# Optimization experiments

Hardware: AMD Instinct MI355X
Metric: run time of the kernel (lower is better)

The kernel has to match this reference:

```python
import jax, jax.numpy as jnp
import numpy as np

N_HEAD = 16
LORA_DIM = 16
LORA_ALPHA = 32


def setup_inputs() -> dict:
    key = jax.random.key(0)
    ks = jax.random.split(key, 8)
    B, S, D = 2, 2048, 1024
    std = 0.02
    return {
        "x": jax.random.normal(ks[0], (B, S, D), jnp.float32),
        "c_attn_w": jax.random.normal(ks[1], (D, 3 * D), jnp.float32) * std,
        "c_attn_b": jnp.zeros((3 * D,), jnp.float32),
        "c_proj_w": jax.random.normal(ks[2], (D, D), jnp.float32) * std,
        "c_proj_b": jnp.zeros((D,), jnp.float32),
        "q_a1": jax.random.normal(ks[3], (D, LORA_DIM), jnp.float32) * std,
        "q_a2": jax.random.normal(ks[4], (LORA_DIM, D), jnp.float32) * std,
        "v_a1": jax.random.normal(ks[5], (D, LORA_DIM), jnp.float32) * std,
        "v_a2": jax.random.normal(ks[6], (LORA_DIM, D), jnp.float32) * std,
    }


def reference(x, c_attn_w, c_attn_b, c_proj_w, c_proj_b, q_a1, q_a2, v_a1, v_a2):
    B, S, D = x.shape
    H = N_HEAD
    hd = D // H
    # NOTE: original code uses adapter_dim / adapter_alpha as the scale
    lora_scale = jnp.float32(LORA_DIM / LORA_ALPHA)

    qkv = x @ c_attn_w + c_attn_b                      # [B,S,3D]
    q, k, v = jnp.split(qkv, 3, axis=-1)
    q = q + ((x @ q_a1) @ q_a2) * lora_scale
    v = v + ((x @ v_a1) @ v_a2) * lora_scale

    def heads(t):
        return t.reshape(B, S, H, hd).transpose(0, 2, 1, 3)  # [B,H,S,hd]

    qh, kh, vh = heads(q), heads(k), heads(v)

    w = jnp.einsum('bhqd,bhkd->bhqk', qh, kh) / jnp.sqrt(jnp.float32(hd))
    bias = jnp.tril(jnp.ones((S, S), dtype=w.dtype))   # causal mask
    w = w * bias - jnp.float32(1e10) * (1 - bias)
    w = jax.nn.softmax(w, axis=-1)
    a = jnp.einsum('bhqk,bhkd->bhqd', w, vh)
    a = a.transpose(0, 2, 1, 3).reshape(B, S, D)       # merge heads
    a = a @ c_proj_w + c_proj_b

    present = jnp.stack((kh, vh))                      # [2,B,H,S,hd]
    return a, present
```

## Files before the change

### kernel.cpp

```cpp
#include <hip/hip_runtime.h>

#define T_TOK 4096
#define D_DIM 1024
#define N3    3072
#define S_LEN 2048
#define NH    16
#define HD    64
#define KAUG  1056

#define OUT_A_ELEMS   4194304
#define OUT_KV_ELEMS  4194304

typedef __attribute__((ext_vector_type(8))) short bf16x8;
typedef __attribute__((ext_vector_type(4))) float f32x4;
typedef __attribute__((ext_vector_type(16))) float f32x16;
typedef _Float16 f16x8 __attribute__((ext_vector_type(8)));
typedef _Float16 f16x4 __attribute__((ext_vector_type(4)));

union U4 { unsigned u[4]; bf16x8 v; };

#define GHASH(r) ((((r) >> 1) ^ ((r) >> 3)) & 3)

__device__ __forceinline__ unsigned short f2bf(float f) {
    unsigned u = __float_as_uint(f);
    u += 0x7FFFu + ((u >> 16) & 1u);
    return (unsigned short)(u >> 16);
}
__device__ __forceinline__ float bf2f(unsigned short h) {
    return __uint_as_float(((unsigned)h) << 16);
}
__device__ __forceinline__ unsigned cvtpk(float a, float b) {
    unsigned r;
    asm("v_cvt_pk_bf16_f32 %0, %1, %2" : "=v"(r) : "v"(a), "v"(b));
    return r;
}

#define GLL16(gp, lp) __builtin_amdgcn_global_load_lds( \
    (const __attribute__((address_space(1))) unsigned int*)(gp), \
    (__attribute__((address_space(3))) unsigned int*)(lp), 16, 0, 0)

#define MFMA32(A, B, C) __builtin_amdgcn_mfma_f32_32x32x16_bf16(A, B, C, 0, 0, 0)
#define MFMA16F(A, B, C) __builtin_amdgcn_mfma_f32_16x16x32_f16(A, B, C, 0, 0, 0)

__global__ __launch_bounds__(256) void lora1_v2(const float* __restrict__ x,
    const float* __restrict__ qa1, const float* __restrict__ va1,
    float* __restrict__ tq, float* __restrict__ tv) {
    int tid = threadIdx.x;
    int w = tid >> 6;
    int lane = tid & 63;
    int t = blockIdx.x * 4 + w;
    int cg = lane & 7;
    int ks = lane >> 3;
    const float* a1 = (cg < 4) ? qa1 : va1;
    int c4 = (cg & 3) * 4;
    const float* xr = x + (size_t)t * D_DIM + ks * 128;
    const float* ar = a1 + (size_t)(ks * 128) * 16 + c4;
    float4 acc = make_float4(0.f, 0.f, 0.f, 0.f);
#pragma unroll 8
    for (int j = 0; j < 128; ++j) {
        float xv = xr[j];
        float4 av = *(const float4*)&ar[j * 16];
        acc.x = fmaf(xv, av.x, acc.x);
        acc.y = fmaf(xv, av.y, acc.y);
        acc.z = fmaf(xv, av.z, acc.z);
        acc.w = fmaf(xv, av.w, acc.w);
    }
#pragma unroll
    for (int m = 8; m < 64; m <<= 1) {
        acc.x += __shfl_xor(acc.x, m);
        acc.y += __shfl_xor(acc.y, m);
        acc.z += __shfl_xor(acc.z, m);
        acc.w += __shfl_xor(acc.w, m);
    }
    if (lane < 8) {
        float* dst = (cg < 4) ? &tq[t * 16 + c4] : &tv[t * 16 + (cg - 4) * 4];
        *(float4*)dst = acc;
    }
}

__global__ __launch_bounds__(256) void splitA_f16(const float* __restrict__ x,
    const float* __restrict__ tq, const float* __restrict__ tv,
    _Float16* __restrict__ af) {
    int idx = blockIdx.x * 256 + threadIdx.x;
    const int total = T_TOK * (KAUG / 4);
    if (idx >= total) return;
    int t = idx / (KAUG / 4);
    int c4 = (idx - t * (KAUG / 4)) * 4;
    float4 v;
    if (c4 < D_DIM)           v = *(const float4*)&x[(size_t)t * D_DIM + c4];
    else if (c4 < D_DIM + 16) v = *(const float4*)&tq[t * 16 + (c4 - D_DIM)];
    else                      v = *(const float4*)&tv[t * 16 + (c4 - D_DIM - 16)];
    f16x4 h;
    h[0] = (_Float16)v.x; h[1] = (_Float16)v.y;
    h[2] = (_Float16)v.z; h[3] = (_Float16)v.w;
    *(f16x4*)&af[(size_t)t * KAUG + c4] = h;
}

__global__ __launch_bounds__(256) void splitW_f16(const float* __restrict__ w,
    const float* __restrict__ qa2, const float* __restrict__ va2,
    _Float16* __restrict__ bf) {
    __shared__ float T[32][65];
    int bn = blockIdx.x;
    int bk = blockIdx.y;
    int tid = threadIdx.x;
#pragma unroll
    for (int u = 0; u < 2; ++u) {
        int id = tid + 256 * u;
        int kr = id >> 4;
        int n4 = (id & 15) * 4;
        int k = bk * 32 + kr;
        int n = bn * 64 + n4;
        float4 v = make_float4(0.f, 0.f, 0.f, 0.f);
        if (k < D_DIM) {
            v = *(const float4*)&w[(size_t)k * N3 + n];
        } else if (k < D_DIM + 16) {
            if (n < D_DIM) {
                float4 q4 = *(const float4*)&qa2[(k - D_DIM) * D_DIM + n];
                v = make_float4(q4.x * 0.5f, q4.y * 0.5f, q4.z * 0.5f, q4.w * 0.5f);
            }
        } else {
            if (n >= 2 * D_DIM) {
                float4 q4 = *(const float4*)&va2[(k - D_DIM - 16) * D_DIM + (n - 2 * D_DIM)];
                v = make_float4(q4.x * 0.5f, q4.y * 0.5f, q4.z * 0.5f, q4.w * 0.5f);
            }
        }
        T[kr][n4 + 0] = v.x; T[kr][n4 + 1] = v.y;
        T[kr][n4 + 2] = v.z; T[kr][n4 + 3] = v.w;
    }
    __syncthreads();
    int n = tid >> 2;
    int k8 = (tid & 3) * 8;
    f16x8 hv;
#pragma unroll
    for (int j = 0; j < 8; ++j) hv[j] = (_Float16)T[k8 + j][n];
    int nr = bn * 64 + n;
    int gsw = (tid & 3) ^ GHASH(nr);
    size_t ro = (size_t)nr * KAUG + bk * 32 + gsw * 8;
    *(f16x8*)&bf[ro] = hv;
}

__global__ __launch_bounds__(256) void wprep_f16(const float* __restrict__ w,
    _Float16* __restrict__ bf) {
    __shared__ float T[32][65];
    int bn = blockIdx.x;
    int bk = blockIdx.y;
    int tid = threadIdx.x;
#pragma unroll
    for (int u = 0; u < 2; ++u) {
        int id = tid + 256 * u;
        int kr = id >> 4;
        int n4 = (id & 15) * 4;
        float4 v = *(const float4*)&w[(size_t)(bk * 32 + kr) * D_DIM + bn * 64 + n4];
        T[kr][n4 + 0] = v.x; T[kr][n4 + 1] = v.y;
        T[kr][n4 + 2] = v.z; T[kr][n4 + 3] = v.w;
    }
    __syncthreads();
    int n = tid >> 2;
    int k8 = (tid & 3) * 8;
    f16x8 hv;
#pragma unroll
    for (int j = 0; j < 8; ++j) hv[j] = (_Float16)T[k8 + j][n];
    int nr = bn * 64 + n;
    int gsw = (tid & 3) ^ GHASH(nr);
    size_t ro = (size_t)nr * D_DIM + bk * 32 + gsw * 8;
    *(f16x8*)&bf[ro] = hv;
}

__global__ __launch_bounds__(256, 3) void qkv_mfma(
    const _Float16* __restrict__ a_g, const _Float16* __restrict__ b_g,
    const float* __restrict__ bias,
    float* __restrict__ qstage, float* __restrict__ pres) {
    __shared__ _Float16 Bf[2][128 * 32];
    int id = blockIdx.y * 24 + blockIdx.x;
    int nid = (id & 7) * 96 + (id >> 3);
    int bn = nid % 24;
    int bm = nid / 24;
    int tid = threadIdx.x;
    int w = tid >> 6, l = tid & 63;
    int wr = w >> 1, wc = w & 1;

    f32x4 acc[4][4];
#pragma unroll
    for (int i = 0; i < 4; ++i)
#pragma unroll
        for (int j = 0; j < 4; ++j)
            acc[i][j] = (f32x4){0.f, 0.f, 0.f, 0.f};

    int srow = l >> 2;
    int sk = (l & 3) * 8;
    const size_t b_base0 = (size_t)(bn * 128 + w * 32 + srow) * KAUG + sk;
    const size_t b_base1 = b_base0 + (size_t)16 * KAUG;
    const int ldso0 = (w * 32) * 32;
    const int ldso1 = (w * 32 + 16) * 32;

    int lrow = l & 15;
    int lg = l >> 4;

    const _Float16* aF[4];
#pragma unroll
    for (int i = 0; i < 4; ++i) {
        int row = bm * 128 + wr * 64 + i * 16 + lrow;
        aF[i] = a_g + (size_t)row * KAUG + lg * 8;
    }
    int roB[4];
#pragma unroll
    for (int j = 0; j < 4; ++j) {
        int Rb = wc * 64 + j * 16 + lrow;
        roB[j] = Rb * 32 + ((lg ^ GHASH(Rb)) * 8);
    }

    f16x8 cA[4], nA[4];

    GLL16(b_g + b_base0, &Bf[0][ldso0]);
    GLL16(b_g + b_base1, &Bf[0][ldso1]);
#pragma unroll
    for (int i = 0; i < 4; ++i) cA[i] = *(const f16x8*)(aF[i]);
    asm volatile("s_waitcnt vmcnt(0)" ::: "memory");
    __builtin_amdgcn_s_barrier();

    const int NT = KAUG / 32;
    for (int t = 0; t < NT; ++t) {
        int cur = t & 1;
        if (t + 1 < NT) {
            int kn = (t + 1) * 32;
            GLL16(b_g + b_base0 + kn, &Bf[cur ^ 1][ldso0]);
            GLL16(b_g + b_base1 + kn, &Bf[cur ^ 1][ldso1]);
            __builtin_amdgcn_sched_barrier(0);
#pragma unroll
            for (int i = 0; i < 4; ++i) nA[i] = *(const f16x8*)(aF[i] + kn);
        }
        f16x8 fb[4];
#pragma unroll
        for (int j = 0; j < 4; ++j) fb[j] = *(const f16x8*)&Bf[cur][roB[j]];
#pragma unroll
        for (int i = 0; i < 4; ++i)
#pragma unroll
            for (int j = 0; j < 4; ++j)
                acc[i][j] = MFMA16F(cA[i], fb[j], acc[i][j]);
        if (t + 1 < NT) {
            asm volatile("s_waitcnt vmcnt(4)" ::: "memory");
            __builtin_amdgcn_s_barrier();
#pragma unroll
            for (int i = 0; i < 4; ++i) cA[i] = nA[i];
        }
    }

    int seg = bn >> 3;
#pragma unroll
    for (int j = 0; j < 4; ++j) {
        int n = bn * 128 + wc * 64 + j * 16 + lrow;
        float bz = bias[n];
        int h = (n >> 6) & 15;
        int d = n & 63;
#pragma unroll
        for (int i = 0; i < 4; ++i) {
            int tbase = bm * 128 + wr * 64 + i * 16 + (l >> 4) * 4;
#pragma unroll
            for (int r = 0; r < 4; ++r) {
                int t = tbase + r;
                float v = acc[i][j][r] + bz;
                int bb = t >> 11, s = t & 2047;
                size_t idx = (((size_t)(bb * NH + h) * S_LEN + s) * HD) + d;
                if (seg == 0)      qstage[idx] = v * 0.125f;
                else if (seg == 1) pres[idx] = v;
                else               pres[OUT_KV_ELEMS + idx] = v;
            }
        }
    }
}

__global__ __launch_bounds__(256, 3) void proj_mfma(
    const _Float16* __restrict__ a_g, const _Float16* __restrict__ b_g,
    const float* __restrict__ bias, float* __restrict__ outp) {
    __shared__ _Float16 Bf[2][128 * 32];
    int id = blockIdx.y * 8 + blockIdx.x;
    int nid = (id & 7) * 32 + (id >> 3);
    int bn = nid % 8;
    int bm = nid / 8;
    int tid = threadIdx.x;
    int w = tid >> 6, l = tid & 63;
    int wr = w >> 1, wc = w & 1;

    f32x4 acc[4][4];
#pragma unroll
    for (int i = 0; i < 4; ++i)
#pragma unroll
        for (int j = 0; j < 4; ++j)
            acc[i][j] = (f32x4){0.f, 0.f, 0.f, 0.f};

    int srow = l >> 2;
    int sk = (l & 3) * 8;
    const size_t b_base0 = (size_t)(bn * 128 + w * 32 + srow) * D_DIM + sk;
    const size_t b_base1 = b_base0 + (size_t)16 * D_DIM;
    const int ldso0 = (w * 32) * 32;
    const int ldso1 = (w * 32 + 16) * 32;

    int lrow = l & 15;
    int lg = l >> 4;

    const _Float16* aF[4];
#pragma unroll
    for (int i = 0; i < 4; ++i) {
        int row = bm * 128 + wr * 64 + i * 16 + lrow;
        aF[i] = a_g + (size_t)row * D_DIM + lg * 8;
    }
    int roB[4];
#pragma unroll
    for (int j = 0; j < 4; ++j) {
        int Rb = wc * 64 + j * 16 + lrow;
        roB[j] = Rb * 32 + ((lg ^ GHASH(Rb)) * 8);
    }

    f16x8 cA[4], nA[4];

    GLL16(b_g + b_base0, &Bf[0][ldso0]);
    GLL16(b_g + b_base1, &Bf[0][ldso1]);
#pragma unroll
    for (int i = 0; i < 4; ++i) cA[i] = *(const f16x8*)(aF[i]);
    asm volatile("s_waitcnt vmcnt(0)" ::: "memory");
    __builtin_amdgcn_s_barrier();

    const int NT = D_DIM / 32;
    for (int t = 0; t < NT; ++t) {
        int cur = t & 1;
        if (t + 1 < NT) {
            int kn = (t + 1) * 32;
            GLL16(b_g + b_base0 + kn, &Bf[cur ^ 1][ldso0]);
            GLL16(b_g + b_base1 + kn, &Bf[cur ^ 1][ldso1]);
            __builtin_amdgcn_sched_barrier(0);
#pragma unroll
            for (int i = 0; i < 4; ++i) nA[i] = *(const f16x8*)(aF[i] + kn);
        }
        f16x8 fb[4];
#pragma unroll
        for (int j = 0; j < 4; ++j) fb[j] = *(const f16x8*)&Bf[cur][roB[j]];
#pragma unroll
        for (int i = 0; i < 4; ++i)
#pragma unroll
            for (int j = 0; j < 4; ++j)
                acc[i][j] = MFMA16F(cA[i], fb[j], acc[i][j]);
        if (t + 1 < NT) {
            asm volatile("s_waitcnt vmcnt(4)" ::: "memory");
            __builtin_amdgcn_s_barrier();
#pragma unroll
            for (int i = 0; i < 4; ++i) cA[i] = nA[i];
        }
    }

#pragma unroll
    for (int j = 0; j < 4; ++j) {
        int n = bn * 128 + wc * 64 + j * 16 + lrow;
        float bz = bias[n];
#pragma unroll
        for (int i = 0; i < 4; ++i) {
            int tbase = bm * 128 + wr * 64 + i * 16 + (l >> 4) * 4;
#pragma unroll
            for (int r = 0; r < 4; ++r)
                outp[(size_t)(tbase + r) * D_DIM + n] = acc[i][j][r] + bz;
        }
    }
}

__global__ __launch_bounds__(256) void kprep_kernel(const float* __restrict__ kin,
    unsigned short* __restrict__ khp, unsigned short* __restrict__ klp) {
    int id = blockIdx.x * 256 + threadIdx.x;
    int rowi = id >> 3;
    int gsrc = id & 7;
    const float* src = kin + (size_t)rowi * 64 + gsrc * 8;
    float4 v0 = *(const float4*)src;
    float4 v1 = *(const float4*)(src + 4);
    int key = rowi & 2047;
    int gp = gsrc ^ (key & 7);
    size_t dst = (size_t)rowi * 64 + gp * 8;
    float vv[8] = {v0.x, v0.y, v0.z, v0.w, v1.x, v1.y, v1.z, v1.w};
    bf16x8 h, lo;
#pragma unroll
    for (int j = 0; j < 8; ++j) {
        unsigned short hh = f2bf(vv[j]);
        h[j] = (short)hh;
        lo[j] = (short)f2bf(vv[j] - bf2f(hh));
    }
    *(bf16x8*)&khp[dst] = h;
    *(bf16x8*)&klp[dst] = lo;
}

__global__ __launch_bounds__(256) void vtprep_kernel(const float* __restrict__ vin,
    unsigned short* __restrict__ vth, unsigned short* __restrict__ vtl) {
    __shared__ __align__(16) unsigned short Th[64][72];
    __shared__ __align__(16) unsigned short Tl[64][72];
    int bh = blockIdx.x;
    int kv0 = blockIdx.y * 64;
    int tid = threadIdx.x;
#pragma unroll
    for (int p = 0; p < 4; ++p) {
        int key = (tid >> 4) + 16 * p;
        int d0 = (tid & 15) * 4;
        float4 v = *(const float4*)&vin[((size_t)bh * 2048 + kv0 + key) * 64 + d0];
        float vv[4] = {v.x, v.y, v.z, v.w};
#pragma unroll
        for (int j = 0; j < 4; ++j) {
            unsigned short hh = f2bf(vv[j]);
            Th[d0 + j][key] = hh;
            Tl[d0 + j][key] = f2bf(vv[j] - bf2f(hh));
        }
    }
    __syncthreads();
    int d = tid >> 2;
#pragma unroll
    for (int q = 0; q < 2; ++q) {
        int gg = (tid & 3) + 4 * q;
        int gs = gg ^ (d & 7);
        bf16x8 hv = *(const bf16x8*)&Th[d][gs * 8];
        bf16x8 lv = *(const bf16x8*)&Tl[d][gs * 8];
        size_t dst = ((size_t)bh * 64 + d) * 2048 + kv0 + gg * 8;
        *(bf16x8*)&vth[dst] = hv;
        *(bf16x8*)&vtl[dst] = lv;
    }
}

__device__ __forceinline__ void stage_tile(
    const unsigned short* __restrict__ kh, const unsigned short* __restrict__ kl,
    const unsigned short* __restrict__ vh, const unsigned short* __restrict__ vl,
    unsigned short (*ldsb)[4096], int w, int l, int bh, int kv0) {
    if (w < 2) {
        const unsigned short* gp = (w == 0 ? kh : kl)
            + ((size_t)bh * 2048 + kv0 + (l >> 3)) * 64 + (l & 7) * 8;
        unsigned short* lp = ldsb[w];
#pragma unroll
        for (int i = 0; i < 8; ++i)
            GLL16(gp + i * 512, lp + i * 512);
    } else {
        const unsigned short* gp = (w == 2 ? vh : vl)
            + ((size_t)bh * 64 + (l >> 3)) * 2048 + kv0 + (l & 7) * 8;
        unsigned short* lp = ldsb[w];
#pragma unroll
        for (int i = 0; i < 8; ++i)
            GLL16(gp + (size_t)i * 16384, lp + i * 512);
    }
}

#define QROW(r) ((((r) & 3) + 8 * ((r) >> 2)) + 4 * g)

__global__ __launch_bounds__(256, 2) void attn_mfma(
    const float* __restrict__ q_s,
    const unsigned short* __restrict__ kh, const unsigned short* __restrict__ kl,
    const unsigned short* __restrict__ vh, const unsigned short* __restrict__ vl,
    _Float16* __restrict__ aout) {
    __shared__ __align__(16) unsigned short lds[2][4][4096];
    int bh = blockIdx.x;
    int qi = (int)gridDim.y - 1 - blockIdx.y;
    int tid = threadIdx.x;
    int w = tid >> 6, l = tid & 63;
    int qloc = l & 31, g = l >> 5;
    int q0 = qi * 128;
    int qg = q0 + w * 32 + qloc;

    bf16x8 qf[4];
    {
        const float* qrow = q_s + ((size_t)bh * S_LEN + qg) * HD;
#pragma unroll
        for (int t = 0; t < 4; ++t) {
            float4 u0 = *(const float4*)&qrow[t * 16 + g * 8];
            float4 u1 = *(const float4*)&qrow[t * 16 + g * 8 + 4];
            float vv[8] = {u0.x, u0.y, u0.z, u0.w, u1.x, u1.y, u1.z, u1.w};
            bf16x8 r;
#pragma unroll
            for (int j = 0; j < 8; ++j) r[j] = (short)f2bf(vv[j]);
            qf[t] = r;
        }
    }

    f32x16 o0, o1;
#pragma unroll
    for (int r = 0; r < 16; ++r) { o0[r] = 0.f; o1[r] = 0.f; }
    float m_run = -1e30f, l_run = 0.f;

    int nt = 2 * qi + 2;
    int qwmax = q0 + w * 32 + 31;

    stage_tile(kh, kl, vh, vl, lds[0], w, l, bh, 0);
    __syncthreads();

    for (int t = 0; t < nt; ++t) {
        int kv0 = t * 64;
        int bi = t & 1;
        if (t + 1 < nt)
            stage_tile(kh, kl, vh, vl, lds[bi ^ 1], w, l, bh, (t + 1) * 64);

        if (kv0 <= qwmax) {
            const unsigned short* Khp = lds[bi][0];
            const unsigned short* Klp = lds[bi][1];
            const unsigned short* Vhp = lds[bi][2];
            const unsigned short* Vlp = lds[bi][3];

            f32x16 s0, s1;
#pragma unroll
            for (int r = 0; r < 16; ++r) { s0[r] = 0.f; s1[r] = 0.f; }

            __builtin_amdgcn_s_setprio(1);
#pragma unroll
            for (int tt = 0; tt < 4; ++tt) {
                int gr = ((2 * tt + g) ^ (qloc & 7)) * 8;
                bf16x8 a0h = *(const bf16x8*)&Khp[qloc * 64 + gr];
                bf16x8 a1h = *(const bf16x8*)&Khp[(32 + qloc) * 64 + gr];
                bf16x8 a0l = *(const bf16x8*)&Klp[qloc * 64 + gr];
                bf16x8 a1l = *(const bf16x8*)&Klp[(32 + qloc) * 64 + gr];
                s0 = MFMA32(a0h, qf[tt], s0);
                s0 = MFMA32(a0l, qf[tt], s0);
                s1 = MFMA32(a1h, qf[tt], s1);
                s1 = MFMA32(a1l, qf[tt], s1);
            }
            __builtin_amdgcn_s_setprio(0);

            if (kv0 + 63 > q0 + w * 32) {
#pragma unroll
                for (int r = 0; r < 16; ++r) {
                    int kk = kv0 + QROW(r);
                    if (kk > qg)      s0[r] = -1e30f;
                    if (kk + 32 > qg) s1[r] = -1e30f;
                }
            }

            float mx = s0[0];
#pragma unroll
            for (int r = 1; r < 16; ++r) mx = fmaxf(mx, s0[r]);
#pragma unroll
            for (int r = 0; r < 16; ++r) mx = fmaxf(mx, s1[r]);
            mx = fmaxf(mx, __shfl_xor(mx, 32));
            float mnew = fmaxf(m_run, mx);
            float al = __expf(m_run - mnew);
            m_run = mnew;
            float rs = 0.f;
#pragma unroll
            for (int r = 0; r < 16; ++r) { s0[r] = __expf(s0[r] - mnew); rs += s0[r]; }
#pragma unroll
            for (int r = 0; r < 16; ++r) { s1[r] = __expf(s1[r] - mnew); rs += s1[r]; }
            rs += __shfl_xor(rs, 32);
            l_run = l_run * al + rs;
#pragma unroll
            for (int r = 0; r < 16; ++r) {
                float ar = __shfl(al, QROW(r));
                o0[r] *= ar; o1[r] *= ar;
            }

            __builtin_amdgcn_s_setprio(1);
#pragma unroll
            for (int ks = 0; ks < 4; ++ks) {
                const int b = (ks & 1) * 8;
                unsigned w0, w1, w2, w3;
                if (ks < 2) {
                    w0 = cvtpk(s0[b + 0], s0[b + 1]);
                    w1 = cvtpk(s0[b + 2], s0[b + 3]);
                    w2 = cvtpk(s0[b + 4], s0[b + 5]);
                    w3 = cvtpk(s0[b + 6], s0[b + 7]);
                } else {
                    w0 = cvtpk(s1[b + 0], s1[b + 1]);
                    w1 = cvtpk(s1[b + 2], s1[b + 3]);
                    w2 = cvtpk(s1[b + 4], s1[b + 5]);
                    w3 = cvtpk(s1[b + 6], s1[b + 7]);
                }
                asm("v_permlane32_swap_b32 %0, %1" : "+v"(w0), "+v"(w2));
                asm("v_permlane32_swap_b32 %0, %1" : "+v"(w1), "+v"(w3));
                U4 u; u.u[0] = w0; u.u[1] = w1; u.u[2] = w2; u.u[3] = w3;
                bf16x8 pa = u.v;
                int gr = ((2 * ks + g) ^ (qloc & 7)) * 8;
                bf16x8 v0h = *(const bf16x8*)&Vhp[qloc * 64 + gr];
                bf16x8 v1h = *(const bf16x8*)&Vhp[(32 + qloc) * 64 + gr];
                bf16x8 v0l = *(const bf16x8*)&Vlp[qloc * 64 + gr];
                bf16x8 v1l = *(const bf16x8*)&Vlp[(32 + qloc) * 64 + gr];
                o0 = MFMA32(pa, v0h, o0);
                o0 = MFMA32(pa, v0l, o0);
                o1 = MFMA32(pa, v1h, o1);
                o1 = MFMA32(pa, v1l, o1);
            }
            __builtin_amdgcn_s_setprio(0);
        }
        __syncthreads();
    }

    int bb = bh >> 4, h = bh & 15;
#pragma unroll
    for (int r = 0; r < 16; ++r) {
        float li = __shfl(l_run, QROW(r));
        float inv = 1.f / li;
        int qq = q0 + w * 32 + QROW(r);
        size_t base = ((size_t)(bb * S_LEN + qq)) * D_DIM + h * HD + qloc;
        aout[base]      = (_Float16)(o0[r] * inv);
        aout[base + 32] = (_Float16)(o1[r] * inv);
    }
}

#define LSTR 68
__global__ __launch_bounds__(256) void attn_kernel(const float* __restrict__ q_s,
    const float* __restrict__ k_s, const float* __restrict__ v_s,
    float* __restrict__ a_s) {
    __shared__ float Qt[64][LSTR];
    __shared__ float KP[64][LSTR];
    __shared__ float Vs[64][LSTR];
    int bh = blockIdx.x;
    int qi = 31 - blockIdx.y;
    int tid = threadIdx.x;
    int tx = tid & 15, ty = tid >> 4;

#pragma unroll
    for (int qq = 0; qq < 4; ++qq) {
        int q  = qq * 16 + (tid >> 4);
        int d4 = (tid & 15) * 4;
        float4 v = *(const float4*)&q_s[((size_t)bh * S_LEN + qi * 64 + q) * HD + d4];
        Qt[d4 + 0][q] = v.x; Qt[d4 + 1][q] = v.y;
        Qt[d4 + 2][q] = v.z; Qt[d4 + 3][q] = v.w;
    }

    float o[4][4];
#pragma unroll
    for (int r = 0; r < 4; ++r)
#pragma unroll
        for (int c = 0; c < 4; ++c) o[r][c] = 0.f;
    float mrow[4] = {-1e30f, -1e30f, -1e30f, -1e30f};
    float lrow[4] = {0.f, 0.f, 0.f, 0.f};

    for (int kt = 0; kt <= qi; ++kt) {
        __syncthreads();
#pragma unroll
        for (int kk2 = 0; kk2 < 4; ++kk2) {
            int k  = kk2 * 16 + (tid >> 4);
            int d4 = (tid & 15) * 4;
            size_t rowoff = ((size_t)bh * S_LEN + kt * 64 + k) * HD + d4;
            float4 kv4 = *(const float4*)&k_s[rowoff];
            KP[d4 + 0][k] = kv4.x; KP[d4 + 1][k] = kv4.y;
            KP[d4 + 2][k] = kv4.z; KP[d4 + 3][k] = kv4.w;
            float4 vv4 = *(const float4*)&v_s[rowoff];
            *(float4*)&Vs[k][d4] = vv4;
        }
        __syncthreads();

        float s[4][4];
#pragma unroll
        for (int r = 0; r < 4; ++r)
#pragma unroll
            for (int c = 0; c < 4; ++c) s[r][c] = 0.f;
#pragma unroll 8
        for (int d = 0; d < 64; ++d) {
            float4 qv = *(const float4*)&Qt[d][ty * 4];
            float4 kv = *(const float4*)&KP[d][tx * 4];
            float qa[4] = {qv.x, qv.y, qv.z, qv.w};
            float ka[4] = {kv.x, kv.y, kv.z, kv.w};
#pragma unroll
            for (int r = 0; r < 4; ++r)
#pragma unroll
                for (int c = 0; c < 4; ++c)
                    s[r][c] = fmaf(qa[r], ka[c], s[r][c]);
        }
        if (kt == qi) {
#pragma unroll
            for (int r = 0; r < 4; ++r)
#pragma unroll
                for (int c = 0; c < 4; ++c)
                    if (tx * 4 + c > ty * 4 + r) s[r][c] = -1e30f;
        }
        __syncthreads();

        float p[4][4];
#pragma unroll
        for (int r = 0; r < 4; ++r) {
            float mx = fmaxf(fmaxf(s[r][0], s[r][1]), fmaxf(s[r][2], s[r][3]));
            mx = fmaxf(mx, __shfl_xor(mx, 1));
            mx = fmaxf(mx, __shfl_xor(mx, 2));
            mx = fmaxf(mx, __shfl_xor(mx, 4));
            mx = fmaxf(mx, __shfl_xor(mx, 8));
            float mn = fmaxf(mrow[r], mx);
            float alpha = __expf(mrow[r] - mn);
            mrow[r] = mn;
            float rsum = 0.f;
#pragma unroll
            for (int c = 0; c < 4; ++c) {
                p[r][c] = __expf(s[r][c] - mn);
                rsum += p[r][c];
            }
            rsum += __shfl_xor(rsum, 1);
            rsum += __shfl_xor(rsum, 2);
            rsum += __shfl_xor(rsum, 4);
            rsum += __shfl_xor(rsum, 8);
            lrow[r] = lrow[r] * alpha + rsum;
#pragma unroll
            for (int c = 0; c < 4; ++c) o[r][c] *= alpha;
            *(float4*)&KP[ty * 4 + r][tx * 4] =
                make_float4(p[r][0], p[r][1], p[r][2], p[r][3]);
        }
        __syncthreads();

#pragma unroll 8
        for (int k = 0; k < 64; ++k) {
            float4 vv = *(const float4*)&Vs[k][tx * 4];
            float va[4] = {vv.x, vv.y, vv.z, vv.w};
#pragma unroll
            for (int r = 0; r < 4; ++r) {
                float pr = KP[ty * 4 + r][k];
#pragma unroll
                for (int c = 0; c < 4; ++c)
                    o[r][c] = fmaf(pr, va[c], o[r][c]);
            }
        }
    }

    int b = bh >> 4, h = bh & 15;
#pragma unroll
    for (int r = 0; r < 4; ++r) {
        int i = qi * 64 + ty * 4 + r;
        float inv = 1.f / lrow[r];
        *(float4*)&a_s[((size_t)(b * S_LEN + i)) * D_DIM + h * HD + tx * 4] =
            make_float4(o[r][0] * inv, o[r][1] * inv, o[r][2] * inv, o[r][3] * inv);
    }
}

__global__ __launch_bounds__(256) void proj_kernel(const float* __restrict__ A,
    const float* __restrict__ w, const float* __restrict__ bias,
    float* __restrict__ outp) {
    __shared__ float As[128][17];
    __shared__ float Bs[16][64];
    int bx = blockIdx.x;
    int by = blockIdx.y;
    int tid = threadIdx.x;
    int tx = tid & 15, ty = tid >> 4;

    float c[8][4];
#pragma unroll
    for (int i = 0; i < 8; ++i)
#pragma unroll
        for (int j = 0; j < 4; ++j) c[i][j] = 0.f;

    for (int k0 = 0; k0 < D_DIM; k0 += 16) {
#pragma unroll
        for (int u = 0; u < 2; ++u) {
            int f4 = tid + 256 * u;
            int row = f4 >> 2;
            int kk4 = (f4 & 3) * 4;
            float4 av = *(const float4*)&A[(size_t)(by * 128 + row) * D_DIM + k0 + kk4];
            As[row][kk4 + 0] = av.x; As[row][kk4 + 1] = av.y;
            As[row][kk4 + 2] = av.z; As[row][kk4 + 3] = av.w;
        }
        {
            int kkb = tid >> 4;
            int col4 = (tid & 15) * 4;
            *(float4*)&Bs[kkb][col4] =
                *(const float4*)&w[(size_t)(k0 + kkb) * D_DIM + bx * 64 + col4];
        }
        __syncthreads();
#pragma unroll
        for (int kk = 0; kk < 16; ++kk) {
            float4 bv = *(const float4*)&Bs[kk][tx * 4];
#pragma unroll
            for (int i = 0; i < 8; ++i) {
                float a = As[ty * 8 + i][kk];
                c[i][0] = fmaf(a, bv.x, c[i][0]);
                c[i][1] = fmaf(a, bv.y, c[i][1]);
                c[i][2] = fmaf(a, bv.z, c[i][2]);
                c[i][3] = fmaf(a, bv.w, c[i][3]);
            }
        }
        __syncthreads();
    }

    int ncol = bx * 64 + tx * 4;
    float4 bias4 = *(const float4*)&bias[ncol];
#pragma unroll
    for (int i = 0; i < 8; ++i) {
        int t = by * 128 + ty * 8 + i;
        *(float4*)&outp[(size_t)t * D_DIM + ncol] =
            make_float4(c[i][0] + bias4.x, c[i][1] + bias4.y,
                        c[i][2] + bias4.z, c[i][3] + bias4.w);
    }
}

extern "C" void kernel_launch(void* const* d_in, const int* in_sizes, int n_in,
                              void* d_out, int out_size, void* d_ws, size_t ws_size,
                              hipStream_t stream) {
    const float* x        = (const float*)d_in[0];
    const float* c_attn_w = (const float*)d_in[1];
    const float* c_attn_b = (const float*)d_in[2];
    const float* c_proj_w = (const float*)d_in[3];
    const float* c_proj_b = (const float*)d_in[4];
    const float* q_a1     = (const float*)d_in[5];
    const float* q_a2     = (const float*)d_in[6];
    const float* v_a1     = (const float*)d_in[7];
    const float* v_a2     = (const float*)d_in[8];

    float* outf   = (float*)d_out;
    float* qstage = outf;
    float* pres   = outf + OUT_A_ELEMS;

    char* wsb = (char*)d_ws;
    float* tq = (float*)wsb;
    float* tv = (float*)(wsb + 262144);
    _Float16* w_f16  = (_Float16*)(wsb + 524288);
    _Float16* a_f16  = (_Float16*)(wsb + 7012352);
    unsigned short* kp_h = (unsigned short*)(wsb + 16777216);
    unsigned short* kp_l = (unsigned short*)(wsb + 25165824);
    unsigned short* vt_h = (unsigned short*)(wsb + 33554432);
    unsigned short* vt_l = (unsigned short*)(wsb + 41943040);
    _Float16* aout_f16 = (_Float16*)wsb;
    _Float16* wp_f16   = (_Float16*)(wsb + 8388608);
    const size_t WS_FULL = 50331648;
    const size_t WS_MID  = 16777216;

    lora1_v2<<<dim3(1024), dim3(256), 0, stream>>>(x, q_a1, v_a1, tq, tv);

    if (ws_size >= WS_FULL) {
        splitA_f16<<<dim3((T_TOK * (KAUG / 4) + 255) / 256), dim3(256), 0, stream>>>(
            x, tq, tv, a_f16);
        splitW_f16<<<dim3(48, KAUG / 32), dim3(256), 0, stream>>>(
            c_attn_w, q_a2, v_a2, w_f16);
        qkv_mfma<<<dim3(24, 32), dim3(256), 0, stream>>>(
            a_f16, w_f16, c_attn_b, qstage, pres);
        kprep_kernel<<<dim3(2048), dim3(256), 0, stream>>>(pres, kp_h, kp_l);
        vtprep_kernel<<<dim3(32, 32), dim3(256), 0, stream>>>(
            pres + OUT_KV_ELEMS, vt_h, vt_l);
        attn_mfma<<<dim3(32, 16), dim3(256), 0, stream>>>(
            qstage, kp_h, kp_l, vt_h, vt_l, aout_f16);
        wprep_f16<<<dim3(16, 32), dim3(256), 0, stream>>>(c_proj_w, wp_f16);
        proj_mfma<<<dim3(8, 32), dim3(256), 0, stream>>>(
            aout_f16, wp_f16, c_proj_b, outf);
    } else if (ws_size >= WS_MID) {
        float* a_s = (float*)wsb;
        splitA_f16<<<dim3((T_TOK * (KAUG / 4) + 255) / 256), dim3(256), 0, stream>>>(
            x, tq, tv, a_f16);
        splitW_f16<<<dim3(48, KAUG / 32), dim3(256), 0, stream>>>(
            c_attn_w, q_a2, v_a2, w_f16);
        qkv_mfma<<<dim3(24, 32), dim3(256), 0, stream>>>(
            a_f16, w_f16, c_attn_b, qstage, pres);
        attn_kernel<<<dim3(32, 32), dim3(256), 0, stream>>>(
            qstage, pres, pres + OUT_KV_ELEMS, a_s);
        proj_kernel<<<dim3(16, 32), dim3(256), 0, stream>>>(
            a_s, c_proj_w, c_proj_b, outf);
    } else {
        float* a_s2 = tv + 65536;
        splitA_f16<<<dim3(1), dim3(1), 0, stream>>>(x, tq, tv, (_Float16*)wsb);
        attn_kernel<<<dim3(32, 32), dim3(256), 0, stream>>>(
            qstage, pres, pres + OUT_KV_ELEMS, a_s2);
        proj_kernel<<<dim3(16, 32), dim3(256), 0, stream>>>(
            a_s2, c_proj_w, c_proj_b, outf);
    }
}
```

Baseline: 284.8 us.

## Switch attention to single-pass fp16 MFMA instead of split bf16 hi/lo

Replaces the bf16 hi+lo split representation of K and V (two MFMAs per product) with a single fp16 copy, halving MFMA count, LDS staging and the prep kernels' memory traffic. The LDS buffer shrinks to half, and launch bounds are raised to allow 4 blocks per CU. P and Q are also converted to fp16 (round-toward-zero pack for P). This trades some precision for speed, and the smaller workspace threshold makes the fast path qualify more often. It also drops a stray one-thread launch in the fallback path.

```diff
diff --git a/kernel.cpp b/kernel.cpp
--- a/kernel.cpp
+++ b/kernel.cpp
@@ -17,7 +17,7 @@
 typedef _Float16 f16x8 __attribute__((ext_vector_type(8)));
 typedef _Float16 f16x4 __attribute__((ext_vector_type(4)));
 
-union U4 { unsigned u[4]; bf16x8 v; };
+union U4h { unsigned u[4]; f16x8 v; };
 
 #define GHASH(r) ((((r) >> 1) ^ ((r) >> 3)) & 3)
 
@@ -29,9 +29,9 @@
 __device__ __forceinline__ float bf2f(unsigned short h) {
     return __uint_as_float(((unsigned)h) << 16);
 }
-__device__ __forceinline__ unsigned cvtpk(float a, float b) {
+__device__ __forceinline__ unsigned cvtpkh(float a, float b) {
     unsigned r;
-    asm("v_cvt_pk_bf16_f32 %0, %1, %2" : "=v"(r) : "v"(a), "v"(b));
+    asm("v_cvt_pkrtz_f16_f32 %0, %1, %2" : "=v"(r) : "v"(a), "v"(b));
     return r;
 }
 
@@ -39,8 +39,8 @@
     (const __attribute__((address_space(1))) unsigned int*)(gp), \
     (__attribute__((address_space(3))) unsigned int*)(lp), 16, 0, 0)
 
-#define MFMA32(A, B, C) __builtin_amdgcn_mfma_f32_32x32x16_bf16(A, B, C, 0, 0, 0)
 #define MFMA16F(A, B, C) __builtin_amdgcn_mfma_f32_16x16x32_f16(A, B, C, 0, 0, 0)
+#define MFMA32F(A, B, C) __builtin_amdgcn_mfma_f32_32x32x16_f16(A, B, C, 0, 0, 0)
 
 __global__ __launch_bounds__(256) void lora1_v2(const float* __restrict__ x,
     const float* __restrict__ qa1, const float* __restrict__ va1,
@@ -361,8 +361,8 @@
     }
 }
 
-__global__ __launch_bounds__(256) void kprep_kernel(const float* __restrict__ kin,
-    unsigned short* __restrict__ khp, unsigned short* __restrict__ klp) {
+__global__ __launch_bounds__(256) void kprep_f16(const float* __restrict__ kin,
+    _Float16* __restrict__ kp) {
     int id = blockIdx.x * 256 + threadIdx.x;
     int rowi = id >> 3;
     int gsrc = id & 7;
@@ -371,23 +371,16 @@
     float4 v1 = *(const float4*)(src + 4);
     int key = rowi & 2047;
     int gp = gsrc ^ (key & 7);
-    size_t dst = (size_t)rowi * 64 + gp * 8;
     float vv[8] = {v0.x, v0.y, v0.z, v0.w, v1.x, v1.y, v1.z, v1.w};
-    bf16x8 h, lo;
-#pragma unroll
-    for (int j = 0; j < 8; ++j) {
-        unsigned short hh = f2bf(vv[j]);
-        h[j] = (short)hh;
-        lo[j] = (short)f2bf(vv[j] - bf2f(hh));
-    }
-    *(bf16x8*)&khp[dst] = h;
-    *(bf16x8*)&klp[dst] = lo;
-}
-
-__global__ __launch_bounds__(256) void vtprep_kernel(const float* __restrict__ vin,
-    unsigned short* __restrict__ vth, unsigned short* __restrict__ vtl) {
-    __shared__ __align__(16) unsigned short Th[64][72];
-    __shared__ __align__(16) unsigned short Tl[64][72];
+    f16x8 h;
+#pragma unroll
+    for (int j = 0; j < 8; ++j) h[j] = (_Float16)vv[j];
+    *(f16x8*)&kp[(size_t)rowi * 64 + gp * 8] = h;
+}
+
+__global__ __launch_bounds__(256) void vtprep_f16(const float* __restrict__ vin,
+    _Float16* __restrict__ vt) {
+    __shared__ __align__(16) _Float16 T[64][72];
     int bh = blockIdx.x;
     int kv0 = blockIdx.y * 64;
     int tid = threadIdx.x;
@@ -396,13 +389,10 @@
         int key = (tid >> 4) + 16 * p;
         int d0 = (tid & 15) * 4;
         float4 v = *(const float4*)&vin[((size_t)bh * 2048 + kv0 + key) * 64 + d0];
-        float vv[4] = {v.x, v.y, v.z, v.w};
-#pragma unroll
-        for (int j = 0; j < 4; ++j) {
-            unsigned short hh = f2bf(vv[j]);
-            Th[d0 + j][key] = hh;
-            Tl[d0 + j][key] = f2bf(vv[j] - bf2f(hh));
-        }
+        T[d0 + 0][key] = (_Float16)v.x;
+        T[d0 + 1][key] = (_Float16)v.y;
+        T[d0 + 2][key] = (_Float16)v.z;
+        T[d0 + 3][key] = (_Float16)v.w;
     }
     __syncthreads();
     int d = tid >> 2;
@@ -410,43 +400,40 @@
     for (int q = 0; q < 2; ++q) {
         int gg = (tid & 3) + 4 * q;
         int gs = gg ^ (d & 7);
-        bf16x8 hv = *(const bf16x8*)&Th[d][gs * 8];
-        bf16x8 lv = *(const bf16x8*)&Tl[d][gs * 8];
+        f16x8 hv = *(const f16x8*)&T[d][gs * 8];
         size_t dst = ((size_t)bh * 64 + d) * 2048 + kv0 + gg * 8;
-        *(bf16x8*)&vth[dst] = hv;
-        *(bf16x8*)&vtl[dst] = lv;
+        *(f16x8*)&vt[dst] = hv;
     }
 }
 
 __device__ __forceinline__ void stage_tile(
-    const unsigned short* __restrict__ kh, const unsigned short* __restrict__ kl,
-    const unsigned short* __restrict__ vh, const unsigned short* __restrict__ vl,
-    unsigned short (*ldsb)[4096], int w, int l, int bh, int kv0) {
+    const _Float16* __restrict__ kp, const _Float16* __restrict__ vt,
+    _Float16 (*ldsb)[4096], int w, int l, int bh, int kv0) {
     if (w < 2) {
-        const unsigned short* gp = (w == 0 ? kh : kl)
-            + ((size_t)bh * 2048 + kv0 + (l >> 3)) * 64 + (l & 7) * 8;
-        unsigned short* lp = ldsb[w];
-#pragma unroll
-        for (int i = 0; i < 8; ++i)
+        const _Float16* gp = kp
+            + ((size_t)bh * 2048 + kv0 + w * 32 + (l >> 3)) * 64 + (l & 7) * 8;
+        _Float16* lp = ldsb[0] + (w * 32) * 64;
+#pragma unroll
+        for (int i = 0; i < 4; ++i)
             GLL16(gp + i * 512, lp + i * 512);
     } else {
-        const unsigned short* gp = (w == 2 ? vh : vl)
-            + ((size_t)bh * 64 + (l >> 3)) * 2048 + kv0 + (l & 7) * 8;
-        unsigned short* lp = ldsb[w];
-#pragma unroll
-        for (int i = 0; i < 8; ++i)
-            GLL16(gp + (size_t)i * 16384, lp + i * 512);
+        int wv = w - 2;
+        const _Float16* gp = vt
+            + ((size_t)bh * 64 + wv * 32 + (l >> 3)) * 2048 + kv0 + (l & 7) * 8;
+        _Float16* lp = ldsb[1] + (wv * 32) * 64;
+#pragma unroll
+        for (int i = 0; i < 4; ++i)
+            GLL16(gp + (size_t)i * 8 * 2048, lp + i * 512);
     }
 }
 
 #define QROW(r) ((((r) & 3) + 8 * ((r) >> 2)) + 4 * g)
 
-__global__ __launch_bounds__(256, 2) void attn_mfma(
+__global__ __launch_bounds__(256, 4) void attn_mfma(
     const float* __restrict__ q_s,
-    const unsigned short* __restrict__ kh, const unsigned short* __restrict__ kl,
-    const unsigned short* __restrict__ vh, const unsigned short* __restrict__ vl,
+    const _Float16* __restrict__ kp, const _Float16* __restrict__ vt,
     _Float16* __restrict__ aout) {
-    __shared__ __align__(16) unsigned short lds[2][4][4096];
+    __shared__ __align__(16) _Float16 lds[2][2][4096];
     int bh = blockIdx.x;
     int qi = (int)gridDim.y - 1 - blockIdx.y;
     int tid = threadIdx.x;
@@ -455,17 +442,15 @@
     int q0 = qi * 128;
     int qg = q0 + w * 32 + qloc;
 
-    bf16x8 qf[4];
+    f16x8 qf[4];
     {
         const float* qrow = q_s + ((size_t)bh * S_LEN + qg) * HD;
 #pragma unroll
         for (int t = 0; t < 4; ++t) {
-            float4 u0 = *(const float4*)&qrow[t * 16 + g * 8];
-            float4 u1 = *(const float4*)&qrow[t * 16 + g * 8 + 4];
-            float vv[8] = {u0.x, u0.y, u0.z, u0.w, u1.x, u1.y, u1.z, u1.w};
-            bf16x8 r;
-#pragma unroll
-            for (int j = 0; j < 8; ++j) r[j] = (short)f2bf(vv[j]);
+            f16x8 r;
+#pragma unroll
+            for (int j = 0; j < 8; ++j)
+                r[j] = (_Float16)qrow[t * 16 + g * 8 + j];
             qf[t] = r;
         }
     }
@@ -478,20 +463,18 @@
     int nt = 2 * qi + 2;
     int qwmax = q0 + w * 32 + 31;
 
-    stage_tile(kh, kl, vh, vl, lds[0], w, l, bh, 0);
+    stage_tile(kp, vt, lds[0], w, l, bh, 0);
     __syncthreads();
 
     for (int t = 0; t < nt; ++t) {
         int kv0 = t * 64;
         int bi = t & 1;
         if (t + 1 < nt)
-            stage_tile(kh, kl, vh, vl, lds[bi ^ 1], w, l, bh, (t + 1) * 64);
+            stage_tile(kp, vt, lds[bi ^ 1], w, l, bh, (t + 1) * 64);
 
         if (kv0 <= qwmax) {
-            const unsigned short* Khp = lds[bi][0];
-            const unsigned short* Klp = lds[bi][1];
-            const unsigned short* Vhp = lds[bi][2];
-            const unsigned short* Vlp = lds[bi][3];
+            const _Float16* Kp = lds[bi][0];
+            const _Float16* Vp = lds[bi][1];
 
             f32x16 s0, s1;
 #pragma unroll
@@ -501,14 +484,10 @@
 #pragma unroll
             for (int tt = 0; tt < 4; ++tt) {
                 int gr = ((2 * tt + g) ^ (qloc & 7)) * 8;
-                bf16x8 a0h = *(const bf16x8*)&Khp[qloc * 64 + gr];
-                bf16x8 a1h = *(const bf16x8*)&Khp[(32 + qloc) * 64 + gr];
-                bf16x8 a0l = *(const bf16x8*)&Klp[qloc * 64 + gr];
-                bf16x8 a1l = *(const bf16x8*)&Klp[(32 + qloc) * 64 + gr];
-                s0 = MFMA32(a0h, qf[tt], s0);
-                s0 = MFMA32(a0l, qf[tt], s0);
-                s1 = MFMA32(a1h, qf[tt], s1);
-                s1 = MFMA32(a1l, qf[tt], s1);
+                f16x8 a0 = *(const f16x8*)&Kp[qloc * 64 + gr];
+                f16x8 a1 = *(const f16x8*)&Kp[(32 + qloc) * 64 + gr];
+                s0 = MFMA32F(a0, qf[tt], s0);
+                s1 = MFMA32F(a1, qf[tt], s1);
             }
             __builtin_amdgcn_s_setprio(0);
 
@@ -549,29 +528,25 @@
                 const int b = (ks & 1) * 8;
                 unsigned w0, w1, w2, w3;
                 if (ks < 2) {
-                    w0 = cvtpk(s0[b + 0], s0[b + 1]);
-                    w1 = cvtpk(s0[b + 2], s0[b + 3]);
-                    w2 = cvtpk(s0[b + 4], s0[b + 5]);
-                    w3 = cvtpk(s0[b + 6], s0[b + 7]);
+                    w0 = cvtpkh(s0[b + 0], s0[b + 1]);
+                    w1 = cvtpkh(s0[b + 2], s0[b + 3]);
+                    w2 = cvtpkh(s0[b + 4], s0[b + 5]);
+                    w3 = cvtpkh(s0[b + 6], s0[b + 7]);
                 } else {
-                    w0 = cvtpk(s1[b + 0], s1[b + 1]);
-                    w1 = cvtpk(s1[b + 2], s1[b + 3]);
-                    w2 = cvtpk(s1[b + 4], s1[b + 5]);
-                    w3 = cvtpk(s1[b + 6], s1[b + 7]);
+                    w0 = cvtpkh(s1[b + 0], s1[b + 1]);
+                    w1 = cvtpkh(s1[b + 2], s1[b + 3]);
+                    w2 = cvtpkh(s1[b + 4], s1[b + 5]);
+                    w3 = cvtpkh(s1[b + 6], s1[b + 7]);
                 }
                 asm("v_permlane32_swap_b32 %0, %1" : "+v"(w0), "+v"(w2));
                 asm("v_permlane32_swap_b32 %0, %1" : "+v"(w1), "+v"(w3));
-                U4 u; u.u[0] = w0; u.u[1] = w1; u.u[2] = w2; u.u[3] = w3;
-                bf16x8 pa = u.v;
+                U4h u; u.u[0] = w0; u.u[1] = w1; u.u[2] = w2; u.u[3] = w3;
+                f16x8 pa = u.v;
                 int gr = ((2 * ks + g) ^ (qloc & 7)) * 8;
-                bf16x8 v0h = *(const bf16x8*)&Vhp[qloc * 64 + gr];
-                bf16x8 v1h = *(const bf16x8*)&Vhp[(32 + qloc) * 64 + gr];
-                bf16x8 v0l = *(const bf16x8*)&Vlp[qloc * 64 + gr];
-                bf16x8 v1l = *(const bf16x8*)&Vlp[(32 + qloc) * 64 + gr];
-                o0 = MFMA32(pa, v0h, o0);
-                o0 = MFMA32(pa, v0l, o0);
-                o1 = MFMA32(pa, v1h, o1);
-                o1 = MFMA32(pa, v1l, o1);
+                f16x8 v0 = *(const f16x8*)&Vp[qloc * 64 + gr];
+                f16x8 v1 = *(const f16x8*)&Vp[(32 + qloc) * 64 + gr];
+                o0 = MFMA32F(pa, v0, o0);
+                o1 = MFMA32F(pa, v1, o1);
             }
             __builtin_amdgcn_s_setprio(0);
         }
@@ -794,13 +769,11 @@
     float* tv = (float*)(wsb + 262144);
     _Float16* w_f16  = (_Float16*)(wsb + 524288);
     _Float16* a_f16  = (_Float16*)(wsb + 7012352);
-    unsigned short* kp_h = (unsigned short*)(wsb + 16777216);
-    unsigned short* kp_l = (unsigned short*)(wsb + 25165824);
-    unsigned short* vt_h = (unsigned short*)(wsb + 33554432);
-    unsigned short* vt_l = (unsigned short*)(wsb + 41943040);
+    _Float16* kp_f16 = (_Float16*)(wsb + 16777216);
+    _Float16* vt_f16 = (_Float16*)(wsb + 25165824);
     _Float16* aout_f16 = (_Float16*)wsb;
     _Float16* wp_f16   = (_Float16*)(wsb + 8388608);
-    const size_t WS_FULL = 50331648;
+    const size_t WS_FULL = 33554432;
     const size_t WS_MID  = 16777216;
 
     lora1_v2<<<dim3(1024), dim3(256), 0, stream>>>(x, q_a1, v_a1, tq, tv);
@@ -812,11 +785,11 @@
             c_attn_w, q_a2, v_a2, w_f16);
         qkv_mfma<<<dim3(24, 32), dim3(256), 0, stream>>>(
             a_f16, w_f16, c_attn_b, qstage, pres);
-        kprep_kernel<<<dim3(2048), dim3(256), 0, stream>>>(pres, kp_h, kp_l);
-        vtprep_kernel<<<dim3(32, 32), dim3(256), 0, stream>>>(
-            pres + OUT_KV_ELEMS, vt_h, vt_l);
+        kprep_f16<<<dim3(2048), dim3(256), 0, stream>>>(pres, kp_f16);
+        vtprep_f16<<<dim3(32, 32), dim3(256), 0, stream>>>(
+            pres + OUT_KV_ELEMS, vt_f16);
         attn_mfma<<<dim3(32, 16), dim3(256), 0, stream>>>(
-            qstage, kp_h, kp_l, vt_h, vt_l, aout_f16);
+            qstage, kp_f16, vt_f16, aout_f16);
         wprep_f16<<<dim3(16, 32), dim3(256), 0, stream>>>(c_proj_w, wp_f16);
         proj_mfma<<<dim3(8, 32), dim3(256), 0, stream>>>(
             aout_f16, wp_f16, c_proj_b, outf);
@@ -834,7 +807,6 @@
             a_s, c_proj_w, c_proj_b, outf);
     } else {
         float* a_s2 = tv + 65536;
-        splitA_f16<<<dim3(1), dim3(1), 0, stream>>>(x, tq, tv, (_Float16*)wsb);
         attn_kernel<<<dim3(32, 32), dim3(256), 0, stream>>>(
             qstage, pres, pres + OUT_KV_ELEMS, a_s2);
         proj_kernel<<<dim3(16, 32), dim3(256), 0, stream>>>(
```

Result: faster. 260.5 us (-8.5%).
